# Optimization experiments

Hardware: AMD Instinct MI355X
Metric: run time of the kernel (lower is better)

Reference implementation:

```python
import jax, jax.numpy as jnp
import numpy as np
import math

NUM_HEADS = 16
FEATURE_DIM = 512
HIDDEN_DIM = 1024
B, T = 4, 2048


def setup_inputs() -> dict:
    key = jax.random.key(0)
    ks = jax.random.split(key, 10)
    sequence = jax.random.normal(ks[0], (B, T, FEATURE_DIM), dtype=jnp.float32)
    mask = jax.random.randint(ks[1], (B, T), 0, 2, dtype=jnp.int32)
    mask = mask.at[:, 0].set(1)  # guarantee at least one valid key per row
    s = 0.02
    Wq = jax.random.normal(ks[2], (FEATURE_DIM, HIDDEN_DIM), dtype=jnp.float32) * s
    bq = jnp.zeros((HIDDEN_DIM,), dtype=jnp.float32)
    Wk = jax.random.normal(ks[3], (FEATURE_DIM, HIDDEN_DIM), dtype=jnp.float32) * s
    bk = jnp.zeros((HIDDEN_DIM,), dtype=jnp.float32)
    Wv = jax.random.normal(ks[4], (FEATURE_DIM, HIDDEN_DIM), dtype=jnp.float32) * s
    bv = jnp.zeros((HIDDEN_DIM,), dtype=jnp.float32)
    Wo = jax.random.normal(ks[5], (HIDDEN_DIM, HIDDEN_DIM), dtype=jnp.float32) * s
    bo = jnp.zeros((HIDDEN_DIM,), dtype=jnp.float32)
    return {"sequence": sequence, "mask": mask, "Wq": Wq, "bq": bq,
            "Wk": Wk, "bk": bk, "Wv": Wv, "bv": bv, "Wo": Wo, "bo": bo}


def reference(sequence, mask, Wq, bq, Wk, bk, Wv, bv, Wo, bo):
    # sequence: (B, T, D); mask: (B, T) int (nonzero = valid key)
    Bb, Tt, _ = sequence.shape
    H = NUM_HEADS
    Dh = Wq.shape[1] // H
    q = (sequence @ Wq + bq).reshape(Bb, Tt, H, Dh)
    k = (sequence @ Wk + bk).reshape(Bb, Tt, H, Dh)
    v = (sequence @ Wv + bv).reshape(Bb, Tt, H, Dh)
    scores = jnp.einsum('bqhd,bkhd->bhqk', q, k) / math.sqrt(Dh)
    key_mask = (mask != 0)[:, None, None, :]  # (B,1,1,T)
    scores = jnp.where(key_mask, scores, -jnp.inf)
    attn = jax.nn.softmax(scores, axis=-1)
    attn = jnp.nan_to_num(attn, nan=0.0, posinf=0.0, neginf=0.0)
    # dropout is identity in eval mode
    context = jnp.einsum('bhqk,bkhd->bqhd', attn, v).reshape(Bb, Tt, H * Dh)
    out = context @ Wo + bo
    return out, attn
```

## Files before the change

kernel.cpp:

```cpp
#include <hip/hip_runtime.h>
#include <hip/hip_bf16.h>
#include <cstdint>
#include <cstddef>

#define NHEADS 16
#define FEAT   512
#define HID    1024
#define BATCH  4
#define SEQ    2048
#define DH     64
#define BT     (BATCH * SEQ)

typedef __attribute__((ext_vector_type(8))) short short8v;
typedef __attribute__((ext_vector_type(4))) float floatx4;

#define MFMA16(a, b, c) __builtin_amdgcn_mfma_f32_16x16x32_bf16((a), (b), (c), 0, 0, 0)

#define GLOAD16(SRC, DST)                                                        \
  __builtin_amdgcn_global_load_lds(                                              \
      (const __attribute__((address_space(1))) void*)(SRC),                      \
      (__attribute__((address_space(3))) void*)(DST), 16, 0, 0)

__device__ __forceinline__ unsigned short f2bf(float x) {
  unsigned u = __float_as_uint(x);
  return (unsigned short)((u + 0x7fffu + ((u >> 16) & 1u)) >> 16);
}
__device__ __forceinline__ float bf2f(unsigned short b) {
  return __uint_as_float((unsigned)b << 16);
}

__device__ __forceinline__ short8v ldst8(const unsigned short* tile, int row, int cbyte) {
  return *reinterpret_cast<const short8v*>(
      (const char*)tile + row * 128 + (cbyte ^ ((row & 7) << 4)));
}

__global__ __launch_bounds__(256) void cvt_kernel(const float* __restrict__ in,
                                                  unsigned short* __restrict__ out, int n8) {
  int i = blockIdx.x * 256 + threadIdx.x;
  if (i >= n8) return;
  const float4* p = reinterpret_cast<const float4*>(in + (size_t)i * 8);
  float4 a = p[0], b = p[1];
  short8v r;
  r[0] = (short)f2bf(a.x); r[1] = (short)f2bf(a.y);
  r[2] = (short)f2bf(a.z); r[3] = (short)f2bf(a.w);
  r[4] = (short)f2bf(b.x); r[5] = (short)f2bf(b.y);
  r[6] = (short)f2bf(b.z); r[7] = (short)f2bf(b.w);
  *reinterpret_cast<short8v*>(out + (size_t)i * 8) = r;
}

__global__ __launch_bounds__(256) void wt_transpose(const float* __restrict__ W,
                                                    unsigned short* __restrict__ outHi,
                                                    unsigned short* __restrict__ outLo,
                                                    int K, int N) {
  __shared__ float t[64][68];
  const int tid = threadIdx.x;
  const int n0 = blockIdx.x * 64, k0 = blockIdx.y * 64;
#pragma unroll
  for (int i = 0; i < 4; ++i) {
    const int kr = (tid >> 4) + i * 16;
    const float4 v = *reinterpret_cast<const float4*>(
        &W[(size_t)(k0 + kr) * N + n0 + (tid & 15) * 4]);
    t[kr][(tid & 15) * 4 + 0] = v.x;
    t[kr][(tid & 15) * 4 + 1] = v.y;
    t[kr][(tid & 15) * 4 + 2] = v.z;
    t[kr][(tid & 15) * 4 + 3] = v.w;
  }
  __syncthreads();
  const int n = tid >> 2, kb0 = (tid & 3) * 16;
  short8v h0, h1, l0, l1;
#pragma unroll
  for (int jj = 0; jj < 8; ++jj) {
    float v = t[kb0 + jj][n];
    unsigned short hu = f2bf(v);
    h0[jj] = (short)hu;
    l0[jj] = (short)f2bf(v - bf2f(hu));
    v = t[kb0 + 8 + jj][n];
    hu = f2bf(v);
    h1[jj] = (short)hu;
    l1[jj] = (short)f2bf(v - bf2f(hu));
  }
  const size_t o = (size_t)(n0 + n) * K + k0 + kb0;
  *reinterpret_cast<short8v*>(outHi + o) = h0;
  *reinterpret_cast<short8v*>(outHi + o + 8) = h1;
  if (outLo) {
    *reinterpret_cast<short8v*>(outLo + o) = l0;
    *reinterpret_cast<short8v*>(outLo + o + 8) = l1;
  }
}

__global__ __launch_bounds__(256) void v_transpose(const unsigned short* __restrict__ vb,
                                                   unsigned short* __restrict__ vt) {
  __shared__ unsigned short t[64][72];
  const int tid = threadIdx.x;
  const int b = blockIdx.z, h = blockIdx.y, t0 = blockIdx.x * 64;
#pragma unroll
  for (int i = 0; i < 2; ++i) {
    const int tok = (tid >> 3) + i * 32;
    const short8v rv = *reinterpret_cast<const short8v*>(
        vb + (size_t)(b * SEQ + t0 + tok) * HID + h * DH + (tid & 7) * 8);
#pragma unroll
    for (int jj = 0; jj < 8; ++jj) t[tok][(tid & 7) * 8 + jj] = (unsigned short)rv[jj];
  }
  __syncthreads();
  const int d = tid >> 2, tb0 = (tid & 3) * 16;
  short8v r0, r1;
#pragma unroll
  for (int jj = 0; jj < 8; ++jj) {
    r0[jj] = (short)t[tb0 + jj][d];
    r1[jj] = (short)t[tb0 + 8 + jj][d];
  }
  const size_t o = ((size_t)(b * NHEADS + h) * DH + d) * SEQ + t0 + tb0;
  *reinterpret_cast<short8v*>(vt + o) = r0;
  *reinterpret_cast<short8v*>(vt + o + 8) = r1;
}

template <int OUT_MODE>
__global__ __launch_bounds__(256) void gemm_bf16(const unsigned short* __restrict__ A,
                                                 const unsigned short* __restrict__ Bt,
                                                 const float* __restrict__ bias, void* Cv,
                                                 int M, int N, int K) {
  __shared__ __align__(16) unsigned short As[128 * 64];
  __shared__ __align__(16) unsigned short Bs[128 * 64];
  const int tid = threadIdx.x, lane = tid & 63, w = tid >> 6;
  const int lg = lane >> 4, lr = lane & 15;
  const int m0 = blockIdx.x * 128, n0 = blockIdx.y * 128;
  const int wm = (w & 1) * 64, wn = (w >> 1) * 64;

  floatx4 acc[4][4];
#pragma unroll
  for (int i = 0; i < 4; ++i)
#pragma unroll
    for (int j = 0; j < 4; ++j) acc[i][j] = (floatx4){0.f, 0.f, 0.f, 0.f};

  const int cb = ((lane & 7) ^ (lane >> 3)) << 4;
  for (int k0 = 0; k0 < K; k0 += 64) {
    __syncthreads();
#pragma unroll
    for (int i = 0; i < 4; ++i) {
      const int r = w * 8 + i * 32 + (lane >> 3);
      GLOAD16((const char*)(A + (size_t)(m0 + r) * K + k0) + cb,
              (char*)As + w * 1024 + i * 4096);
      GLOAD16((const char*)(Bt + (size_t)(n0 + r) * K + k0) + cb,
              (char*)Bs + w * 1024 + i * 4096);
    }
    __syncthreads();
#pragma unroll
    for (int w2 = 0; w2 < 2; ++w2) {
      short8v af[4], bf[4];
#pragma unroll
      for (int f = 0; f < 4; ++f) {
        af[f] = ldst8(As, wm + f * 16 + lr, w2 * 64 + lg * 16);
        bf[f] = ldst8(Bs, wn + f * 16 + lr, w2 * 64 + lg * 16);
      }
#pragma unroll
      for (int fm = 0; fm < 4; ++fm)
#pragma unroll
        for (int fn = 0; fn < 4; ++fn) acc[fm][fn] = MFMA16(af[fm], bf[fn], acc[fm][fn]);
    }
  }

#pragma unroll
  for (int fm = 0; fm < 4; ++fm) {
    const int row = m0 + wm + fm * 16 + lg * 4;
#pragma unroll
    for (int fn = 0; fn < 4; ++fn) {
      const int col = n0 + wn + fn * 16 + lr;
      if (OUT_MODE == 0) {
        const float bv = bias[col];
        unsigned short* C = (unsigned short*)Cv;
#pragma unroll
        for (int j = 0; j < 4; ++j)
          C[(size_t)(row + j) * N + col] = f2bf(acc[fm][fn][j] + bv);
      } else if (OUT_MODE == 1) {
        const float bv = bias[col];
        float* C = (float*)Cv;
#pragma unroll
        for (int j = 0; j < 4; ++j) C[(size_t)(row + j) * N + col] = acc[fm][fn][j] + bv;
      } else {
        float* C = (float*)Cv;
#pragma unroll
        for (int j = 0; j < 4; ++j) C[(size_t)(row + j) * N + col] += acc[fm][fn][j];
      }
    }
  }
}

__global__ __launch_bounds__(256) void attn_mfma(const unsigned short* __restrict__ qg,
                                                 const unsigned short* __restrict__ kg,
                                                 const unsigned short* __restrict__ vt,
                                                 const int* __restrict__ mask,
                                                 float* __restrict__ attn,
                                                 unsigned short* __restrict__ ctxh,
                                                 unsigned short* __restrict__ ctxl) {
  __shared__ __align__(16) unsigned short Qs[64 * 64];
  __shared__ __align__(16) unsigned short Ks[64 * 64];
  __shared__ __align__(16) unsigned short Vs[64 * 64];
  __shared__ __align__(16) unsigned short Ps[64 * 64];
  __shared__ float mb[SEQ];

  const int tid = threadIdx.x, lane = tid & 63, w = tid >> 6;
  const int lg = lane >> 4, lr = lane & 15;
  const int b = blockIdx.z, h = blockIdx.y, q0 = blockIdx.x * 64;
  const int qw = w * 16;
  const int cb = ((lane & 7) ^ (lane >> 3)) << 4;

  for (int i = tid; i < SEQ; i += 256) mb[i] = mask[b * SEQ + i] ? 0.f : -3.0e38f;

  {
    const unsigned short* g0 = qg + (size_t)(b * SEQ + q0) * HID + h * DH;
#pragma unroll
    for (int i = 0; i < 2; ++i) {
      const int r = w * 8 + i * 32 + (lane >> 3);
      GLOAD16((const char*)(g0 + (size_t)r * HID) + cb, (char*)Qs + w * 1024 + i * 4096);
    }
  }
  __syncthreads();

  short8v qa[2];
  qa[0] = ldst8(Qs, qw + lr, lg * 16);
  qa[1] = ldst8(Qs, qw + lr, 64 + lg * 16);

  const unsigned short* kbase = kg + (size_t)(b * SEQ) * HID + h * DH;
  const unsigned short* vtb = vt + (size_t)(b * NHEADS + h) * DH * SEQ;

  float sums[4] = {0.f, 0.f, 0.f, 0.f};

  for (int k0 = 0; k0 < SEQ; k0 += 64) {
    __syncthreads();
#pragma unroll
    for (int i = 0; i < 2; ++i) {
      const int r = w * 8 + i * 32 + (lane >> 3);
      GLOAD16((const char*)(kbase + (size_t)(k0 + r) * HID) + cb,
              (char*)Ks + w * 1024 + i * 4096);
    }
    __syncthreads();
    floatx4 s[4];
#pragma unroll
    for (int fn = 0; fn < 4; ++fn) s[fn] = (floatx4){0.f, 0.f, 0.f, 0.f};
#pragma unroll
    for (int w2 = 0; w2 < 2; ++w2)
#pragma unroll
      for (int fn = 0; fn < 4; ++fn) {
        const short8v kf = ldst8(Ks, fn * 16 + lr, w2 * 64 + lg * 16);
        s[fn] = MFMA16(qa[w2], kf, s[fn]);
      }
#pragma unroll
    for (int fn = 0; fn < 4; ++fn) {
      const float mbv = mb[k0 + fn * 16 + lr];
#pragma unroll
      for (int j = 0; j < 4; ++j) sums[j] += __expf(fmaf(s[fn][j], 0.125f, mbv));
    }
  }

#pragma unroll
  for (int m = 1; m < 16; m <<= 1)
#pragma unroll
    for (int j = 0; j < 4; ++j) sums[j] += __shfl_xor(sums[j], m, 64);
  float invS[4];
#pragma unroll
  for (int j = 0; j < 4; ++j) invS[j] = 1.f / sums[j];

  floatx4 cacc[4];
#pragma unroll
  for (int fn = 0; fn < 4; ++fn) cacc[fn] = (floatx4){0.f, 0.f, 0.f, 0.f};

  for (int k0 = 0; k0 < SEQ; k0 += 64) {
    __syncthreads();
#pragma unroll
    for (int i = 0; i < 2; ++i) {
      const int r = w * 8 + i * 32 + (lane >> 3);
      GLOAD16((const char*)(kbase + (size_t)(k0 + r) * HID) + cb,
              (char*)Ks + w * 1024 + i * 4096);
      GLOAD16((const char*)(vtb + (size_t)r * SEQ + k0) + cb,
              (char*)Vs + w * 1024 + i * 4096);
    }
    __syncthreads();
    floatx4 s[4];
#pragma unroll
    for (int fn = 0; fn < 4; ++fn) s[fn] = (floatx4){0.f, 0.f, 0.f, 0.f};
#pragma unroll
    for (int w2 = 0; w2 < 2; ++w2)
#pragma unroll
      for (int fn = 0; fn < 4; ++fn) {
        const short8v kf = ldst8(Ks, fn * 16 + lr, w2 * 64 + lg * 16);
        s[fn] = MFMA16(qa[w2], kf, s[fn]);
      }
#pragma unroll
    for (int fn = 0; fn < 4; ++fn) {
      const float mbv = mb[k0 + fn * 16 + lr];
      const int cb0 = (fn * 16 + lr) * 2;
#pragma unroll
      for (int j = 0; j < 4; ++j) {
        const float p = __expf(fmaf(s[fn][j], 0.125f, mbv)) * invS[j];
        const int q = qw + lg * 4 + j;
        *(unsigned short*)((char*)Ps + q * 128 + (cb0 ^ ((q & 7) << 4))) = f2bf(p);
      }
    }
    __syncthreads();

    const short8v pa0 = ldst8(Ps, qw + lr, lg * 16);
    const short8v pa1 = ldst8(Ps, qw + lr, 64 + lg * 16);
#pragma unroll
    for (int fn = 0; fn < 4; ++fn) {
      const short8v v0 = ldst8(Vs, fn * 16 + lr, lg * 16);
      const short8v v1 = ldst8(Vs, fn * 16 + lr, 64 + lg * 16);
      cacc[fn] = MFMA16(pa0, v0, cacc[fn]);
      cacc[fn] = MFMA16(pa1, v1, cacc[fn]);
    }

    {
      const int q = tid >> 2, c16 = (tid & 3) * 16;
      float* arow = attn + ((size_t)((b * NHEADS + h) * SEQ + q0 + q)) * SEQ + k0 + c16;
#pragma unroll
      for (int hp = 0; hp < 2; ++hp) {
        const short8v pv = *reinterpret_cast<const short8v*>(
            (const char*)Ps + q * 128 + (((c16 + hp * 8) * 2) ^ ((q & 7) << 4)));
        float4 o0, o1;
        o0.x = bf2f((unsigned short)pv[0]); o0.y = bf2f((unsigned short)pv[1]);
        o0.z = bf2f((unsigned short)pv[2]); o0.w = bf2f((unsigned short)pv[3]);
        o1.x = bf2f((unsigned short)pv[4]); o1.y = bf2f((unsigned short)pv[5]);
        o1.z = bf2f((unsigned short)pv[6]); o1.w = bf2f((unsigned short)pv[7]);
        *reinterpret_cast<float4*>(arow + hp * 8) = o0;
        *reinterpret_cast<float4*>(arow + hp * 8 + 4) = o1;
      }
    }
  }

#pragma unroll
  for (int fn = 0; fn < 4; ++fn) {
#pragma unroll
    for (int j = 0; j < 4; ++j) {
      const float v = cacc[fn][j];
      const unsigned short hu = f2bf(v);
      const size_t idx =
          (size_t)(b * SEQ + q0 + qw + lg * 4 + j) * HID + h * DH + fn * 16 + lr;
      ctxh[idx] = hu;
      ctxl[idx] = f2bf(v - bf2f(hu));
    }
  }
}

extern "C" void kernel_launch(void* const* d_in, const int* in_sizes, int n_in,
                              void* d_out, int out_size, void* d_ws, size_t ws_size,
                              hipStream_t stream) {
  (void)in_sizes; (void)n_in; (void)out_size; (void)ws_size;

  const float* seq = (const float*)d_in[0];
  const int*   msk = (const int*)d_in[1];
  const float* Wq  = (const float*)d_in[2];
  const float* bq  = (const float*)d_in[3];
  const float* Wk  = (const float*)d_in[4];
  const float* bk  = (const float*)d_in[5];
  const float* Wv  = (const float*)d_in[6];
  const float* bv  = (const float*)d_in[7];
  const float* Wo  = (const float*)d_in[8];
  const float* bo  = (const float*)d_in[9];

  float* out  = (float*)d_out;
  float* attn = out + (size_t)BT * HID;

  unsigned short* p = (unsigned short*)d_ws;
  unsigned short* seqb = p; p += (size_t)BT * FEAT;
  unsigned short* wqt  = p; p += (size_t)HID * FEAT;
  unsigned short* wkt  = p; p += (size_t)HID * FEAT;
  unsigned short* wvt  = p; p += (size_t)HID * FEAT;
  unsigned short* woth = p; p += (size_t)HID * HID;
  unsigned short* wotl = p; p += (size_t)HID * HID;
  unsigned short* qb   = p; p += (size_t)BT * HID;
  unsigned short* kb   = p; p += (size_t)BT * HID;
  unsigned short* vb   = p; p += (size_t)BT * HID;
  unsigned short* vtb  = p; p += (size_t)BT * HID;
  unsigned short* ctxh = p; p += (size_t)BT * HID;
  unsigned short* ctxl = p; p += (size_t)BT * HID;

  cvt_kernel<<<dim3(BT * FEAT / (8 * 256)), dim3(256), 0, stream>>>(seq, seqb, BT * FEAT / 8);
  wt_transpose<<<dim3(HID / 64, FEAT / 64), dim3(256), 0, stream>>>(Wq, wqt, nullptr, FEAT, HID);
  wt_transpose<<<dim3(HID / 64, FEAT / 64), dim3(256), 0, stream>>>(Wk, wkt, nullptr, FEAT, HID);
  wt_transpose<<<dim3(HID / 64, FEAT / 64), dim3(256), 0, stream>>>(Wv, wvt, nullptr, FEAT, HID);
  wt_transpose<<<dim3(HID / 64, HID / 64), dim3(256), 0, stream>>>(Wo, woth, wotl, HID, HID);

  dim3 blk(256), gg(BT / 128, HID / 128);
  gemm_bf16<0><<<gg, blk, 0, stream>>>(seqb, wqt, bq, qb, BT, HID, FEAT);
  gemm_bf16<0><<<gg, blk, 0, stream>>>(seqb, wkt, bk, kb, BT, HID, FEAT);
  gemm_bf16<0><<<gg, blk, 0, stream>>>(seqb, wvt, bv, vb, BT, HID, FEAT);

  v_transpose<<<dim3(SEQ / 64, NHEADS, BATCH), blk, 0, stream>>>(vb, vtb);

  attn_mfma<<<dim3(SEQ / 64, NHEADS, BATCH), blk, 0, stream>>>(qb, kb, vtb, msk, attn,
                                                               ctxh, ctxl);

  gemm_bf16<1><<<gg, blk, 0, stream>>>(ctxh, woth, bo, out, BT, HID, HID);
  gemm_bf16<2><<<gg, blk, 0, stream>>>(ctxh, wotl, nullptr, out, BT, HID, HID);
  gemm_bf16<2><<<gg, blk, 0, stream>>>(ctxl, woth, nullptr, out, BT, HID, HID);
}
```

Measured before the change: 1.547 ms.

## Fuse QKV projections, merge split-precision output GEMMs, widen attention blocks to 128 queries

The three Q/K/V projection GEMMs become one GEMM over a concatenated weight matrix writing an interleaved QKV buffer. The three hi/lo output-projection GEMM passes become one kernel that loads all four operand tiles and accumulates the three MFMA products together, so the fp32 output is no longer read and rewritten. The attention kernel now uses 512 threads covering 128 queries per block, so each loaded K/V tile is shared by twice as many queries. The cost is more LDS per block in the attention and output kernels, which may lower occupancy.

```diff
diff --git a/kernel.cpp b/kernel.cpp
--- a/kernel.cpp
+++ b/kernel.cpp
@@ -6,6 +6,7 @@
 #define NHEADS 16
 #define FEAT   512
 #define HID    1024
+#define QKVN   (3 * HID)
 #define BATCH  4
 #define SEQ    2048
 #define DH     64
@@ -97,7 +98,7 @@
   for (int i = 0; i < 2; ++i) {
     const int tok = (tid >> 3) + i * 32;
     const short8v rv = *reinterpret_cast<const short8v*>(
-        vb + (size_t)(b * SEQ + t0 + tok) * HID + h * DH + (tid & 7) * 8);
+        vb + (size_t)(b * SEQ + t0 + tok) * QKVN + h * DH + (tid & 7) * 8);
 #pragma unroll
     for (int jj = 0; jj < 8; ++jj) t[tok][(tid & 7) * 8 + jj] = (unsigned short)rv[jj];
   }
@@ -114,11 +115,12 @@
   *reinterpret_cast<short8v*>(vt + o + 8) = r1;
 }
 
-template <int OUT_MODE>
-__global__ __launch_bounds__(256) void gemm_bf16(const unsigned short* __restrict__ A,
-                                                 const unsigned short* __restrict__ Bt,
-                                                 const float* __restrict__ bias, void* Cv,
-                                                 int M, int N, int K) {
+__global__ __launch_bounds__(256) void gemm_qkv(const unsigned short* __restrict__ A,
+                                                const unsigned short* __restrict__ Bt,
+                                                const float* __restrict__ b0,
+                                                const float* __restrict__ b1,
+                                                const float* __restrict__ b2,
+                                                unsigned short* __restrict__ C) {
   __shared__ __align__(16) unsigned short As[128 * 64];
   __shared__ __align__(16) unsigned short Bs[128 * 64];
   const int tid = threadIdx.x, lane = tid & 63, w = tid >> 6;
@@ -133,14 +135,14 @@
     for (int j = 0; j < 4; ++j) acc[i][j] = (floatx4){0.f, 0.f, 0.f, 0.f};
 
   const int cb = ((lane & 7) ^ (lane >> 3)) << 4;
-  for (int k0 = 0; k0 < K; k0 += 64) {
+  for (int k0 = 0; k0 < FEAT; k0 += 64) {
     __syncthreads();
 #pragma unroll
     for (int i = 0; i < 4; ++i) {
       const int r = w * 8 + i * 32 + (lane >> 3);
-      GLOAD16((const char*)(A + (size_t)(m0 + r) * K + k0) + cb,
+      GLOAD16((const char*)(A + (size_t)(m0 + r) * FEAT + k0) + cb,
               (char*)As + w * 1024 + i * 4096);
-      GLOAD16((const char*)(Bt + (size_t)(n0 + r) * K + k0) + cb,
+      GLOAD16((const char*)(Bt + (size_t)(n0 + r) * FEAT + k0) + cb,
               (char*)Bs + w * 1024 + i * 4096);
     }
     __syncthreads();
@@ -165,53 +167,112 @@
 #pragma unroll
     for (int fn = 0; fn < 4; ++fn) {
       const int col = n0 + wn + fn * 16 + lr;
-      if (OUT_MODE == 0) {
-        const float bv = bias[col];
-        unsigned short* C = (unsigned short*)Cv;
-#pragma unroll
-        for (int j = 0; j < 4; ++j)
-          C[(size_t)(row + j) * N + col] = f2bf(acc[fm][fn][j] + bv);
-      } else if (OUT_MODE == 1) {
-        const float bv = bias[col];
-        float* C = (float*)Cv;
-#pragma unroll
-        for (int j = 0; j < 4; ++j) C[(size_t)(row + j) * N + col] = acc[fm][fn][j] + bv;
-      } else {
-        float* C = (float*)Cv;
-#pragma unroll
-        for (int j = 0; j < 4; ++j) C[(size_t)(row + j) * N + col] += acc[fm][fn][j];
-      }
-    }
-  }
-}
-
-__global__ __launch_bounds__(256) void attn_mfma(const unsigned short* __restrict__ qg,
+      const float* bp = (col < HID) ? b0 : ((col < 2 * HID) ? b1 : b2);
+      const float bv = bp[col & (HID - 1)];
+#pragma unroll
+      for (int j = 0; j < 4; ++j)
+        C[(size_t)(row + j) * QKVN + col] = f2bf(acc[fm][fn][j] + bv);
+    }
+  }
+}
+
+__global__ __launch_bounds__(256) void gemm_out3(const unsigned short* __restrict__ Ah,
+                                                 const unsigned short* __restrict__ Al,
+                                                 const unsigned short* __restrict__ Bh,
+                                                 const unsigned short* __restrict__ Bl,
+                                                 const float* __restrict__ bias,
+                                                 float* __restrict__ C) {
+  __shared__ __align__(16) unsigned short Ahs[128 * 64];
+  __shared__ __align__(16) unsigned short Als[128 * 64];
+  __shared__ __align__(16) unsigned short Bhs[128 * 64];
+  __shared__ __align__(16) unsigned short Bls[128 * 64];
+  const int tid = threadIdx.x, lane = tid & 63, w = tid >> 6;
+  const int lg = lane >> 4, lr = lane & 15;
+  const int m0 = blockIdx.x * 128, n0 = blockIdx.y * 128;
+  const int wm = (w & 1) * 64, wn = (w >> 1) * 64;
+
+  floatx4 acc[4][4];
+#pragma unroll
+  for (int i = 0; i < 4; ++i)
+#pragma unroll
+    for (int j = 0; j < 4; ++j) acc[i][j] = (floatx4){0.f, 0.f, 0.f, 0.f};
+
+  const int cb = ((lane & 7) ^ (lane >> 3)) << 4;
+  for (int k0 = 0; k0 < HID; k0 += 64) {
+    __syncthreads();
+#pragma unroll
+    for (int i = 0; i < 4; ++i) {
+      const int r = w * 8 + i * 32 + (lane >> 3);
+      const int dst = w * 1024 + i * 4096;
+      GLOAD16((const char*)(Ah + (size_t)(m0 + r) * HID + k0) + cb, (char*)Ahs + dst);
+      GLOAD16((const char*)(Al + (size_t)(m0 + r) * HID + k0) + cb, (char*)Als + dst);
+      GLOAD16((const char*)(Bh + (size_t)(n0 + r) * HID + k0) + cb, (char*)Bhs + dst);
+      GLOAD16((const char*)(Bl + (size_t)(n0 + r) * HID + k0) + cb, (char*)Bls + dst);
+    }
+    __syncthreads();
+#pragma unroll
+    for (int w2 = 0; w2 < 2; ++w2) {
+      short8v ah[4], al[4];
+#pragma unroll
+      for (int f = 0; f < 4; ++f) {
+        ah[f] = ldst8(Ahs, wm + f * 16 + lr, w2 * 64 + lg * 16);
+        al[f] = ldst8(Als, wm + f * 16 + lr, w2 * 64 + lg * 16);
+      }
+#pragma unroll
+      for (int fn = 0; fn < 4; ++fn) {
+        const short8v bh = ldst8(Bhs, wn + fn * 16 + lr, w2 * 64 + lg * 16);
+        const short8v bl = ldst8(Bls, wn + fn * 16 + lr, w2 * 64 + lg * 16);
+#pragma unroll
+        for (int fm = 0; fm < 4; ++fm) {
+          acc[fm][fn] = MFMA16(ah[fm], bh, acc[fm][fn]);
+          acc[fm][fn] = MFMA16(al[fm], bh, acc[fm][fn]);
+          acc[fm][fn] = MFMA16(ah[fm], bl, acc[fm][fn]);
+        }
+      }
+    }
+  }
+
+#pragma unroll
+  for (int fm = 0; fm < 4; ++fm) {
+    const int row = m0 + wm + fm * 16 + lg * 4;
+#pragma unroll
+    for (int fn = 0; fn < 4; ++fn) {
+      const int col = n0 + wn + fn * 16 + lr;
+      const float bv = bias[col];
+#pragma unroll
+      for (int j = 0; j < 4; ++j) C[(size_t)(row + j) * HID + col] = acc[fm][fn][j] + bv;
+    }
+  }
+}
+
+__global__ __launch_bounds__(512) void attn_mfma(const unsigned short* __restrict__ qg,
                                                  const unsigned short* __restrict__ kg,
                                                  const unsigned short* __restrict__ vt,
                                                  const int* __restrict__ mask,
                                                  float* __restrict__ attn,
                                                  unsigned short* __restrict__ ctxh,
                                                  unsigned short* __restrict__ ctxl) {
-  __shared__ __align__(16) unsigned short Qs[64 * 64];
+  __shared__ __align__(16) unsigned short Qs[128 * 64];
   __shared__ __align__(16) unsigned short Ks[64 * 64];
   __shared__ __align__(16) unsigned short Vs[64 * 64];
-  __shared__ __align__(16) unsigned short Ps[64 * 64];
+  __shared__ __align__(16) unsigned short Ps[128 * 64];
   __shared__ float mb[SEQ];
 
   const int tid = threadIdx.x, lane = tid & 63, w = tid >> 6;
   const int lg = lane >> 4, lr = lane & 15;
-  const int b = blockIdx.z, h = blockIdx.y, q0 = blockIdx.x * 64;
+  const int b = blockIdx.z, h = blockIdx.y, q0 = blockIdx.x * 128;
   const int qw = w * 16;
-  const int cb = ((lane & 7) ^ (lane >> 3)) << 4;
-
-  for (int i = tid; i < SEQ; i += 256) mb[i] = mask[b * SEQ + i] ? 0.f : -3.0e38f;
+  const int cb512 = (((tid & 7) ^ ((tid >> 3) & 7)) << 4);
+
+  for (int i = tid; i < SEQ; i += 512) mb[i] = mask[b * SEQ + i] ? 0.f : -3.0e38f;
 
   {
-    const unsigned short* g0 = qg + (size_t)(b * SEQ + q0) * HID + h * DH;
+    const unsigned short* g0 = qg + (size_t)(b * SEQ + q0) * QKVN + h * DH;
 #pragma unroll
     for (int i = 0; i < 2; ++i) {
-      const int r = w * 8 + i * 32 + (lane >> 3);
-      GLOAD16((const char*)(g0 + (size_t)r * HID) + cb, (char*)Qs + w * 1024 + i * 4096);
+      const int r = (tid >> 3) + i * 64;
+      GLOAD16((const char*)(g0 + (size_t)r * QKVN) + cb512,
+              (char*)Qs + w * 1024 + i * 8192);
     }
   }
   __syncthreads();
@@ -220,18 +281,17 @@
   qa[0] = ldst8(Qs, qw + lr, lg * 16);
   qa[1] = ldst8(Qs, qw + lr, 64 + lg * 16);
 
-  const unsigned short* kbase = kg + (size_t)(b * SEQ) * HID + h * DH;
+  const unsigned short* kbase = kg + (size_t)(b * SEQ) * QKVN + h * DH;
   const unsigned short* vtb = vt + (size_t)(b * NHEADS + h) * DH * SEQ;
 
   float sums[4] = {0.f, 0.f, 0.f, 0.f};
 
   for (int k0 = 0; k0 < SEQ; k0 += 64) {
     __syncthreads();
-#pragma unroll
-    for (int i = 0; i < 2; ++i) {
-      const int r = w * 8 + i * 32 + (lane >> 3);
-      GLOAD16((const char*)(kbase + (size_t)(k0 + r) * HID) + cb,
-              (char*)Ks + w * 1024 + i * 4096);
+    {
+      const int r = tid >> 3;
+      GLOAD16((const char*)(kbase + (size_t)(k0 + r) * QKVN) + cb512,
+              (char*)Ks + w * 1024);
     }
     __syncthreads();
     floatx4 s[4];
@@ -266,13 +326,12 @@
 
   for (int k0 = 0; k0 < SEQ; k0 += 64) {
     __syncthreads();
-#pragma unroll
-    for (int i = 0; i < 2; ++i) {
-      const int r = w * 8 + i * 32 + (lane >> 3);
-      GLOAD16((const char*)(kbase + (size_t)(k0 + r) * HID) + cb,
-              (char*)Ks + w * 1024 + i * 4096);
-      GLOAD16((const char*)(vtb + (size_t)r * SEQ + k0) + cb,
-              (char*)Vs + w * 1024 + i * 4096);
+    {
+      const int r = tid >> 3;
+      GLOAD16((const char*)(kbase + (size_t)(k0 + r) * QKVN) + cb512,
+              (char*)Ks + w * 1024);
+      GLOAD16((const char*)(vtb + (size_t)r * SEQ + k0) + cb512,
+              (char*)Vs + w * 1024);
     }
     __syncthreads();
     floatx4 s[4];
@@ -360,36 +419,31 @@
   float* attn = out + (size_t)BT * HID;
 
   unsigned short* p = (unsigned short*)d_ws;
-  unsigned short* seqb = p; p += (size_t)BT * FEAT;
-  unsigned short* wqt  = p; p += (size_t)HID * FEAT;
-  unsigned short* wkt  = p; p += (size_t)HID * FEAT;
-  unsigned short* wvt  = p; p += (size_t)HID * FEAT;
-  unsigned short* woth = p; p += (size_t)HID * HID;
-  unsigned short* wotl = p; p += (size_t)HID * HID;
-  unsigned short* qb   = p; p += (size_t)BT * HID;
-  unsigned short* kb   = p; p += (size_t)BT * HID;
-  unsigned short* vb   = p; p += (size_t)BT * HID;
-  unsigned short* vtb  = p; p += (size_t)BT * HID;
-  unsigned short* ctxh = p; p += (size_t)BT * HID;
-  unsigned short* ctxl = p; p += (size_t)BT * HID;
-
-  cvt_kernel<<<dim3(BT * FEAT / (8 * 256)), dim3(256), 0, stream>>>(seq, seqb, BT * FEAT / 8);
-  wt_transpose<<<dim3(HID / 64, FEAT / 64), dim3(256), 0, stream>>>(Wq, wqt, nullptr, FEAT, HID);
-  wt_transpose<<<dim3(HID / 64, FEAT / 64), dim3(256), 0, stream>>>(Wk, wkt, nullptr, FEAT, HID);
-  wt_transpose<<<dim3(HID / 64, FEAT / 64), dim3(256), 0, stream>>>(Wv, wvt, nullptr, FEAT, HID);
-  wt_transpose<<<dim3(HID / 64, HID / 64), dim3(256), 0, stream>>>(Wo, woth, wotl, HID, HID);
-
-  dim3 blk(256), gg(BT / 128, HID / 128);
-  gemm_bf16<0><<<gg, blk, 0, stream>>>(seqb, wqt, bq, qb, BT, HID, FEAT);
-  gemm_bf16<0><<<gg, blk, 0, stream>>>(seqb, wkt, bk, kb, BT, HID, FEAT);
-  gemm_bf16<0><<<gg, blk, 0, stream>>>(seqb, wvt, bv, vb, BT, HID, FEAT);
-
-  v_transpose<<<dim3(SEQ / 64, NHEADS, BATCH), blk, 0, stream>>>(vb, vtb);
-
-  attn_mfma<<<dim3(SEQ / 64, NHEADS, BATCH), blk, 0, stream>>>(qb, kb, vtb, msk, attn,
-                                                               ctxh, ctxl);
-
-  gemm_bf16<1><<<gg, blk, 0, stream>>>(ctxh, woth, bo, out, BT, HID, HID);
-  gemm_bf16<2><<<gg, blk, 0, stream>>>(ctxh, wotl, nullptr, out, BT, HID, HID);
-  gemm_bf16<2><<<gg, blk, 0, stream>>>(ctxl, woth, nullptr, out, BT, HID, HID);
-}
+  unsigned short* seqb  = p; p += (size_t)BT * FEAT;
+  unsigned short* wqkvt = p; p += (size_t)QKVN * FEAT;
+  unsigned short* woth  = p; p += (size_t)HID * HID;
+  unsigned short* wotl  = p; p += (size_t)HID * HID;
+  unsigned short* qkvb  = p; p += (size_t)BT * QKVN;
+  unsigned short* vtb   = p; p += (size_t)BT * HID;
+  unsigned short* ctxh  = p; p += (size_t)BT * HID;
+  unsigned short* ctxl  = p; p += (size_t)BT * HID;
+
+  dim3 blk(256);
+
+  cvt_kernel<<<dim3(BT * FEAT / (8 * 256)), blk, 0, stream>>>(seq, seqb, BT * FEAT / 8);
+  wt_transpose<<<dim3(HID / 64, FEAT / 64), blk, 0, stream>>>(Wq, wqkvt, nullptr, FEAT, HID);
+  wt_transpose<<<dim3(HID / 64, FEAT / 64), blk, 0, stream>>>(
+      Wk, wqkvt + (size_t)HID * FEAT, nullptr, FEAT, HID);
+  wt_transpose<<<dim3(HID / 64, FEAT / 64), blk, 0, stream>>>(
+      Wv, wqkvt + (size_t)2 * HID * FEAT, nullptr, FEAT, HID);
+  wt_transpose<<<dim3(HID / 64, HID / 64), blk, 0, stream>>>(Wo, woth, wotl, HID, HID);
+
+  gemm_qkv<<<dim3(BT / 128, QKVN / 128), blk, 0, stream>>>(seqb, wqkvt, bq, bk, bv, qkvb);
+
+  v_transpose<<<dim3(SEQ / 64, NHEADS, BATCH), blk, 0, stream>>>(qkvb + 2 * HID, vtb);
+
+  attn_mfma<<<dim3(SEQ / 128, NHEADS, BATCH), dim3(512), 0, stream>>>(
+      qkvb, qkvb + HID, vtb, msk, attn, ctxh, ctxl);
+
+  gemm_out3<<<dim3(BT / 128, HID / 128), blk, 0, stream>>>(ctxh, ctxl, woth, wotl, bo, out);
+}
```

Result: faster. 1.508 ms (-2.6%).
